# Kernel tuning notes

Measured on AMD Instinct MI355X. Metric: run time of the kernel, lower is better.

The kernel has to match this reference:

```python
import jax, jax.numpy as jnp
import numpy as np

INPUT_SIZE = 64
RESERVOIR_SIZE = 2048
SPECTRAL_RADIUS = 0.9
SPARSITY = 0.1
WARMUP = 100
LEAKING_RATE = 0.01
T = 8192


def _make_weights(seed=0):
    rng = np.random.default_rng(seed)
    Win = (rng.random((RESERVOIR_SIZE, INPUT_SIZE)) - 0.5).astype(np.float32)
    Wh = (rng.random((RESERVOIR_SIZE, RESERVOIR_SIZE)) - 0.5).astype(np.float32)
    # scale to spectral radius, then apply sparsity mask (same order as the torch module)
    eig = np.linalg.eigvals(Wh.astype(np.float64))
    Wh = Wh * np.float32(SPECTRAL_RADIUS / np.max(np.abs(eig)))
    mask = (rng.random((RESERVOIR_SIZE, RESERVOIR_SIZE)) < SPARSITY).astype(np.float32)
    Wh = Wh * mask
    return jnp.asarray(Win), jnp.asarray(Wh)


def setup_inputs() -> dict:
    key = jax.random.key(0)
    x = jax.random.normal(key, (T, INPUT_SIZE), dtype=jnp.float32)
    Win, Wh = _make_weights()
    return {"x": x, "Win": Win, "Wh": Wh}


def reference(x, Win, Wh):
    lr = jnp.float32(LEAKING_RATE)

    def step(h, xt):
        h_new = jnp.tanh(Win @ xt + Wh @ h)
        h = (1.0 - lr) * h + lr * h_new
        return h, jnp.concatenate([h, xt])  # extended state [R + I]

    h0 = jnp.zeros((RESERVOIR_SIZE,), dtype=x.dtype)
    _, H_all = jax.lax.scan(step, h0, x)  # [T, R + I]
    return H_all[WARMUP:]                 # [T - warmup, R + I]
```

## Files before the change

### kernel.cpp

```cpp
#include <hip/hip_runtime.h>
#include <hip/hip_fp16.h>
#include <math.h>


#define NWG        128
#define ROWS_PER_WG 16
#define T_STEPS    8192
#define WARMUP     100
#define RSIZE      2048
#define ISIZE      64
#define OUTCOLS    2112
#define MAXREP     8
#define REP_STRIDE_W 16384
#define CAPT       24

#define REP24(F) \
  F(0) F(1) F(2) F(3) F(4) F(5) F(6) F(7) \
  F(8) F(9) F(10) F(11) F(12) F(13) F(14) F(15) \
  F(16) F(17) F(18) F(19) F(20) F(21) F(22) F(23)

#define REP12(F) \
  F(0) F(1) F(2) F(3) F(4) F(5) F(6) F(7) F(8) F(9) F(10) F(11)

#define PAIRS12(F) \
  F(0,0,1) F(1,2,3) F(2,4,5) F(3,6,7) F(4,8,9) F(5,10,11) \
  F(6,12,13) F(7,14,15) F(8,16,17) F(9,18,19) F(10,20,21) F(11,22,23)

#define DECLV(I) float v##I = 0.0f;
#define DECLO(I) unsigned op##I = 0u;
#define SETV(I)  v##I = sv[l * CAPT + (I)];
#define SETO(I)  op##I = (unsigned)si[l * CAPT + 2 * (I)] | ((unsigned)si[l * CAPT + 2 * (I) + 1] << 16);
#define PINV(I)  asm volatile("" : "+v"(v##I));
#define PINO(I)  asm volatile("" : "+v"(op##I));
#define MAC2(P, A, B) \
  if ((A) < cm) { p0 = fmaf(v##A, *(const float*)(hsb + (op##P & 0xFFFFu)), p0); } \
  if ((B) < cm) { p1 = fmaf(v##B, *(const float*)(hsb + (op##P >> 16)),     p1); }

static __device__ __forceinline__ float h16_to_f32(unsigned short u) {
    __half_raw hr; hr.x = u;
    return __half2float(__half(hr));
}
static __device__ __forceinline__ unsigned short f32_to_h16(float f) {
    __half_raw hr = __half_raw(__float2half_rn(f));
    return hr.x;
}

__global__ __launch_bounds__(256) void init_ws_kernel(unsigned* rep0, int nrep) {
    int t = blockIdx.x * blockDim.x + threadIdx.x;
    if (t < nrep * RSIZE) {
        int rep = t >> 11;
        int idx = t & (RSIZE - 1);
        unsigned* b = rep0 + rep * REP_STRIDE_W;
        b[idx]         = 0u;
        b[RSIZE + idx] = 0xFFFF0000u;
    }
}

__global__ __launch_bounds__(256) void xcopy_kernel(const float* __restrict__ x,
                                                    float* __restrict__ out) {
    int t = blockIdx.x * blockDim.x + threadIdx.x;
    if (t >= (T_STEPS - WARMUP) * ISIZE) return;
    int rowo = t >> 6;
    int j    = t & 63;
    out[(size_t)rowo * OUTCOLS + RSIZE + j] = x[(size_t)(rowo + WARMUP) * ISIZE + j];
}

__global__ __launch_bounds__(256, 1) void esn_scan_kernel(
    const float* __restrict__ x,
    const float* __restrict__ Win,
    const float* __restrict__ Wh,
    float* __restrict__ out,
    unsigned* rep0,
    int nrep, int repmask)
{
    __shared__ __align__(16) float hs[RSIZE];
    __shared__ float part[64];
    __shared__ float sv[64 * CAPT];
    __shared__ unsigned short si[64 * CAPT];

    const int tid = threadIdx.x;
    const int wg  = blockIdx.x;
    const int w   = tid >> 6;
    const int l   = tid & 63;
    const int r4  = l >> 2;
    const int c4  = l & 3;
    const int row = wg * ROWS_PER_WG + r4;
    const int seg = w * 512;
    const char* hsb = (const char*)hs;

    const unsigned* myrep = rep0 + (wg & repmask) * REP_STRIDE_W;

    int cnt = 0;
    REP24(DECLV)
    REP12(DECLO)
    const float* wrow = Wh + (size_t)row * RSIZE + seg;
    for (int ph = 0; ph < 4; ++ph) {
        if (w == ph) {
            for (int i = 0; i < CAPT; ++i) { sv[l * CAPT + i] = 0.0f; si[l * CAPT + i] = 0; }
            int c = 0, c2 = 0;
            #pragma unroll 8
            for (int j = 0; j < 512; j += 4) {
                const float4 t4 = *(const float4*)(wrow + j);
                #define TAKE(VAL, COMP) \
                    if ((VAL) != 0.0f) { \
                        if ((c & 3) == c4 && c2 < CAPT) { \
                            sv[l * CAPT + c2] = (VAL); \
                            si[l * CAPT + c2] = (unsigned short)((seg + j + (COMP)) * 4); \
                            ++c2; \
                        } \
                        ++c; \
                    }
                TAKE(t4.x, 0) TAKE(t4.y, 1) TAKE(t4.z, 2) TAKE(t4.w, 3)
                #undef TAKE
            }
            cnt = c2;
            REP24(SETV)
            REP12(SETO)
        }
        __syncthreads();
    }
    REP24(PINV)
    REP12(PINO)

    int cm = cnt;
    #pragma unroll
    for (int d = 1; d < 64; d <<= 1) { const int o = __shfl_xor(cm, d); cm = o > cm ? o : cm; }
    cm = __builtin_amdgcn_readfirstlane(cm);

    float wix, wiy, wiz, wiw;
    { float4 t = *(const float4*)(Win + (size_t)row * ISIZE + w * 16 + c4 * 4);
      wix = t.x; wiy = t.y; wiz = t.z; wiw = t.w; }
    asm volatile("" : "+v"(wix), "+v"(wiy), "+v"(wiz), "+v"(wiw));

    float hcur = 0.0f;

    for (int k = 1; k <= T_STEPS; ++k) {
        const float4 xv = *(const float4*)(x + (size_t)(k - 1) * ISIZE + w * 16 + c4 * 4);

        const unsigned* bp = myrep + (((k - 1) & 1) ? RSIZE : 0) + seg;
        const unsigned long long exp64 =
            ((unsigned long long)(unsigned)(k - 1) << 16) * 0x100000001ull;
        unsigned long long q[4];
        unsigned m = 0xFu;
        while (m) {
#pragma unroll
            for (int s = 0; s < 4; ++s) {
                if (m & (1u << s)) {
                    q[s] = __hip_atomic_load(
                        (const unsigned long long*)(bp + s * 128 + 2 * l),
                        __ATOMIC_RELAXED, __HIP_MEMORY_SCOPE_AGENT);
                }
            }
#pragma unroll
            for (int s = 0; s < 4; ++s) {
                if ((m & (1u << s)) &&
                    (q[s] & 0xFFFF0000FFFF0000ull) == exp64) {
                    m &= ~(1u << s);
                }
            }
        }

#pragma unroll
        for (int s = 0; s < 4; ++s) {
            float2* d = (float2*)(hs + seg + s * 128 + 2 * l);
            float2 v;
            v.x = h16_to_f32((unsigned short)(q[s] & 0xFFFFu));
            v.y = h16_to_f32((unsigned short)((q[s] >> 32) & 0xFFFFu));
            *d = v;
        }

        float p0 = wix * xv.x + wiy * xv.y + wiz * xv.z + wiw * xv.w;
        float p1 = 0.0f;

        PAIRS12(MAC2)

        float p = p0 + p1;
        p += __shfl_xor(p, 1);
        p += __shfl_xor(p, 2);
        if (c4 == 0) part[r4 * 4 + w] = p;

        __syncthreads();

        if (tid < 16) {
            const float4 ps = *(const float4*)(part + tid * 4);
            float y = ps.x + ps.y + ps.z + ps.w;
            float ax = fabsf(y);
            float e  = __expf(2.0f * ax);
            float t  = 1.0f - 2.0f / (e + 1.0f);
            t = copysignf(t, y);
            hcur = 0.99f * hcur + 0.01f * t;

            unsigned word = ((unsigned)k << 16) | (unsigned)f32_to_h16(hcur);
            const int slot = ((k & 1) ? RSIZE : 0) + wg * ROWS_PER_WG + tid;
#pragma unroll
            for (int rr = 0; rr < MAXREP; ++rr) {
                if (rr < nrep) {
                    __hip_atomic_store(rep0 + rr * REP_STRIDE_W + slot, word,
                                       __ATOMIC_RELAXED, __HIP_MEMORY_SCOPE_AGENT);
                }
            }
            if (k >= WARMUP + 1) {
                out[(size_t)(k - (WARMUP + 1)) * OUTCOLS + wg * ROWS_PER_WG + tid] = hcur;
            }
        }
    }
}

extern "C" void kernel_launch(void* const* d_in, const int* in_sizes, int n_in,
                              void* d_out, int out_size, void* d_ws, size_t ws_size,
                              hipStream_t stream) {
    const float* x   = (const float*)d_in[0];
    const float* Win = (const float*)d_in[1];
    const float* Wh  = (const float*)d_in[2];
    float* out = (float*)d_out;

    unsigned* rep0 = (unsigned*)d_ws;

    int nrep = MAXREP;
    while (nrep > 1 && (size_t)nrep * (REP_STRIDE_W * 4) > ws_size) nrep >>= 1;
    int repmask = nrep - 1;

    {
        int n = nrep * RSIZE;
        init_ws_kernel<<<(n + 255) / 256, 256, 0, stream>>>(rep0, nrep);
    }

    {
        int n = (T_STEPS - WARMUP) * ISIZE;
        xcopy_kernel<<<(n + 255) / 256, 256, 0, stream>>>(x, out);
    }

    esn_scan_kernel<<<NWG, 256, 0, stream>>>(x, Win, Wh, out, rep0, nrep, repmask);
}
```

Baseline: 17.34 ms.

## Restructure ESN step loop to overlap polling loads with previous step's tanh and publish

The per-step loop is reordered. The inline-asm global loads for x and the replicated state (with sc0 sc1 cache bypass) are issued first. The previous step's tanh and state publish then run while those loads are in flight. Replica stores are spread across 128 threads, one replica each, instead of 16 threads looping over all replicas, and output writes move to a separate group of threads with nontemporal stores. Polling alternates between double-buffered dwordx4 loads, one contiguous 8-word chunk per thread. Each step still ends with a single barrier. The risks are subtle hand-written waitcnt ordering and the hand-managed cache-bypass semantics.

```diff
diff --git a/kernel.cpp b/kernel.cpp
--- a/kernel.cpp
+++ b/kernel.cpp
@@ -14,6 +14,8 @@
 #define REP_STRIDE_W 16384
 #define CAPT       24
 
+typedef int i32x4 __attribute__((ext_vector_type(4)));
+
 #define REP24(F) \
   F(0) F(1) F(2) F(3) F(4) F(5) F(6) F(7) \
   F(8) F(9) F(10) F(11) F(12) F(13) F(14) F(15) \
@@ -33,8 +35,8 @@
 #define PINV(I)  asm volatile("" : "+v"(v##I));
 #define PINO(I)  asm volatile("" : "+v"(op##I));
 #define MAC2(P, A, B) \
-  if ((A) < cm) { p0 = fmaf(v##A, *(const float*)(hsb + (op##P & 0xFFFFu)), p0); } \
-  if ((B) < cm) { p1 = fmaf(v##B, *(const float*)(hsb + (op##P >> 16)),     p1); }
+  if ((A) < cm) { f0 = fmaf(v##A, *(const float*)(hsb + (op##P & 0xFFFFu)), f0); } \
+  if ((B) < cm) { f1 = fmaf(v##B, *(const float*)(hsb + (op##P >> 16)),     f1); }
 
 static __device__ __forceinline__ float h16_to_f32(unsigned short u) {
     __half_raw hr; hr.x = u;
@@ -132,77 +134,127 @@
       wix = t.x; wiy = t.y; wiz = t.z; wiw = t.w; }
     asm volatile("" : "+v"(wix), "+v"(wiy), "+v"(wiz), "+v"(wiw));
 
+    const int prow = (tid < 128) ? (tid >> 3) : (tid - 128);
     float hcur = 0.0f;
 
+    i32x4 xi, pA, pB, qA, qB;
+
     for (int k = 1; k <= T_STEPS; ++k) {
-        const float4 xv = *(const float4*)(x + (size_t)(k - 1) * ISIZE + w * 16 + c4 * 4);
-
-        const unsigned* bp = myrep + (((k - 1) & 1) ? RSIZE : 0) + seg;
-        const unsigned long long exp64 =
-            ((unsigned long long)(unsigned)(k - 1) << 16) * 0x100000001ull;
-        unsigned long long q[4];
-        unsigned m = 0xFu;
-        while (m) {
-#pragma unroll
-            for (int s = 0; s < 4; ++s) {
-                if (m & (1u << s)) {
-                    q[s] = __hip_atomic_load(
-                        (const unsigned long long*)(bp + s * 128 + 2 * l),
-                        __ATOMIC_RELAXED, __HIP_MEMORY_SCOPE_AGENT);
-                }
-            }
-#pragma unroll
-            for (int s = 0; s < 4; ++s) {
-                if ((m & (1u << s)) &&
-                    (q[s] & 0xFFFF0000FFFF0000ull) == exp64) {
-                    m &= ~(1u << s);
-                }
-            }
-        }
-
-#pragma unroll
-        for (int s = 0; s < 4; ++s) {
-            float2* d = (float2*)(hs + seg + s * 128 + 2 * l);
-            float2 v;
-            v.x = h16_to_f32((unsigned short)(q[s] & 0xFFFFu));
-            v.y = h16_to_f32((unsigned short)((q[s] >> 32) & 0xFFFFu));
-            *d = v;
-        }
-
-        float p0 = wix * xv.x + wiy * xv.y + wiz * xv.z + wiw * xv.w;
-        float p1 = 0.0f;
-
-        PAIRS12(MAC2)
-
-        float p = p0 + p1;
-        p += __shfl_xor(p, 1);
-        p += __shfl_xor(p, 2);
-        if (c4 == 0) part[r4 * 4 + w] = p;
-
-        __syncthreads();
-
-        if (tid < 16) {
-            const float4 ps = *(const float4*)(part + tid * 4);
+        const int psel = ((k - 1) & 1) ? RSIZE : 0;
+        const unsigned* pb = myrep + psel + tid * 8;
+        const float* xp = x + (size_t)(k - 1) * ISIZE + w * 16 + c4 * 4;
+
+        asm volatile(
+            "global_load_dwordx4 %0, %5, off\n\t"
+            "global_load_dwordx4 %1, %6, off sc0 sc1\n\t"
+            "global_load_dwordx4 %2, %6, off offset:16 sc0 sc1\n\t"
+            "global_load_dwordx4 %3, %6, off sc0 sc1\n\t"
+            "global_load_dwordx4 %4, %6, off offset:16 sc0 sc1\n\t"
+            : "=&v"(xi), "=&v"(pA), "=&v"(pB), "=&v"(qA), "=&v"(qB)
+            : "v"(xp), "v"(pb)
+            : "memory");
+
+        if (k > 1 && tid < 144) {
+            const float4 ps = *(const float4*)(part + prow * 4);
             float y = ps.x + ps.y + ps.z + ps.w;
             float ax = fabsf(y);
             float e  = __expf(2.0f * ax);
             float t  = 1.0f - 2.0f / (e + 1.0f);
             t = copysignf(t, y);
             hcur = 0.99f * hcur + 0.01f * t;
-
-            unsigned word = ((unsigned)k << 16) | (unsigned)f32_to_h16(hcur);
-            const int slot = ((k & 1) ? RSIZE : 0) + wg * ROWS_PER_WG + tid;
-#pragma unroll
-            for (int rr = 0; rr < MAXREP; ++rr) {
-                if (rr < nrep) {
-                    __hip_atomic_store(rep0 + rr * REP_STRIDE_W + slot, word,
+            if (tid < 128) {
+                if ((tid & 7) < nrep) {
+                    const unsigned word = ((unsigned)(k - 1) << 16) | (unsigned)f32_to_h16(hcur);
+                    const int slot = psel + wg * ROWS_PER_WG + prow;
+                    __hip_atomic_store(rep0 + (tid & 7) * REP_STRIDE_W + slot, word,
                                        __ATOMIC_RELAXED, __HIP_MEMORY_SCOPE_AGENT);
                 }
-            }
-            if (k >= WARMUP + 1) {
-                out[(size_t)(k - (WARMUP + 1)) * OUTCOLS + wg * ROWS_PER_WG + tid] = hcur;
+            } else if (k - 1 >= WARMUP + 1) {
+                __builtin_nontemporal_store(
+                    hcur, out + (size_t)(k - 1 - (WARMUP + 1)) * OUTCOLS + wg * ROWS_PER_WG + prow);
             }
         }
+
+        asm volatile("s_waitcnt vmcnt(2)"
+                     : "+v"(xi), "+v"(pA), "+v"(pB) :: "memory");
+
+        const unsigned expw = (unsigned)(k - 1) << 16;
+        unsigned dmask = 3u;
+
+        #define CHECK_STAGE(QA, QB) do { \
+            if (dmask & 1u) { \
+                const unsigned d0 = (((unsigned)(QA).x ^ expw) | ((unsigned)(QA).y ^ expw) | \
+                                     ((unsigned)(QA).z ^ expw) | ((unsigned)(QA).w ^ expw)) & 0xFFFF0000u; \
+                if (d0 == 0u) { \
+                    float4 f; \
+                    f.x = h16_to_f32((unsigned short)((QA).x & 0xFFFF)); \
+                    f.y = h16_to_f32((unsigned short)((QA).y & 0xFFFF)); \
+                    f.z = h16_to_f32((unsigned short)((QA).z & 0xFFFF)); \
+                    f.w = h16_to_f32((unsigned short)((QA).w & 0xFFFF)); \
+                    *(float4*)(hs + tid * 8) = f; \
+                    dmask &= ~1u; \
+                } \
+            } \
+            if (dmask & 2u) { \
+                const unsigned d1 = (((unsigned)(QB).x ^ expw) | ((unsigned)(QB).y ^ expw) | \
+                                     ((unsigned)(QB).z ^ expw) | ((unsigned)(QB).w ^ expw)) & 0xFFFF0000u; \
+                if (d1 == 0u) { \
+                    float4 f; \
+                    f.x = h16_to_f32((unsigned short)((QB).x & 0xFFFF)); \
+                    f.y = h16_to_f32((unsigned short)((QB).y & 0xFFFF)); \
+                    f.z = h16_to_f32((unsigned short)((QB).z & 0xFFFF)); \
+                    f.w = h16_to_f32((unsigned short)((QB).w & 0xFFFF)); \
+                    *(float4*)(hs + tid * 8 + 4) = f; \
+                    dmask &= ~2u; \
+                } \
+            } \
+        } while (0)
+
+        #define POLL_ROUND(NA, NB, OA, OB) \
+            asm volatile("global_load_dwordx4 %0, %4, off sc0 sc1\n\t" \
+                         "global_load_dwordx4 %1, %4, off offset:16 sc0 sc1\n\t" \
+                         "s_waitcnt vmcnt(2)" \
+                         : "=&v"(NA), "=&v"(NB), "+v"(OA), "+v"(OB) \
+                         : "v"(pb) : "memory")
+
+        CHECK_STAGE(pA, pB);
+        while (dmask) {
+            POLL_ROUND(pA, pB, qA, qB);
+            CHECK_STAGE(qA, qB);
+            if (!dmask) break;
+            POLL_ROUND(qA, qB, pA, pB);
+            CHECK_STAGE(pA, pB);
+        }
+        #undef POLL_ROUND
+        #undef CHECK_STAGE
+
+        float f0 = wix * __int_as_float(xi.x);
+        f0 = fmaf(wiy, __int_as_float(xi.y), f0);
+        f0 = fmaf(wiz, __int_as_float(xi.z), f0);
+        f0 = fmaf(wiw, __int_as_float(xi.w), f0);
+        float f1 = 0.0f;
+
+        PAIRS12(MAC2)
+
+        float p = f0 + f1;
+        p += __shfl_xor(p, 1);
+        p += __shfl_xor(p, 2);
+        if (c4 == 0) part[r4 * 4 + w] = p;
+
+        asm volatile("s_waitcnt vmcnt(0)" ::: "memory");
+        __syncthreads();
+    }
+
+    if (tid >= 128 && tid < 144) {
+        const float4 ps = *(const float4*)(part + prow * 4);
+        float y = ps.x + ps.y + ps.z + ps.w;
+        float ax = fabsf(y);
+        float e  = __expf(2.0f * ax);
+        float t  = 1.0f - 2.0f / (e + 1.0f);
+        t = copysignf(t, y);
+        hcur = 0.99f * hcur + 0.01f * t;
+        __builtin_nontemporal_store(
+            hcur, out + (size_t)(T_STEPS - (WARMUP + 1)) * OUTCOLS + wg * ROWS_PER_WG + prow);
     }
 }
 
```

Result: slower. 20.37 ms (+17.5%).
